# Optimization experiments

Measured on AMD Instinct MI355X. Metric: run time of the kernel, lower is better.

Reference implementation:

```python
import jax, jax.numpy as jnp
import numpy as np

N = 100000
E = 1600000
IN_C = 128
OUT_C = 32
HEADS = 4
NEG_SLOPE = 0.2


def setup_inputs() -> dict:
    key = jax.random.key(0)
    k1, k2, k3, k4, k5 = jax.random.split(key, 5)
    x = jax.random.normal(k1, (N, IN_C), dtype=jnp.float32)
    edge_index = jax.random.randint(k2, (2, E), 0, N, dtype=jnp.int64)
    # Xavier-ish scaled params
    W = jax.random.normal(k3, (OUT_C * HEADS, IN_C), dtype=jnp.float32) * (1.414 * np.sqrt(2.0 / (IN_C + OUT_C * HEADS)))
    att_l = jax.random.normal(k4, (1, HEADS, OUT_C), dtype=jnp.float32) * 0.1
    att_r = jax.random.normal(k5, (1, HEADS, OUT_C), dtype=jnp.float32) * 0.1
    bias = jnp.zeros((OUT_C * HEADS,), dtype=jnp.float32)
    return {"x": x, "edge_index": edge_index, "W": W, "att_l": att_l, "att_r": att_r, "bias": bias}


def reference(x, edge_index, W, att_l, att_r, bias):
    row, col = edge_index[0], edge_index[1]
    # per-node projection: [N, H, C]
    x_proj = (x @ W.T).reshape(N, HEADS, OUT_C)
    x_i = x_proj[row]          # [E, H, C] gather by source
    x_j = x_proj[col]          # [E, H, C] gather by target
    alpha = (x_i * att_l).sum(-1) + (x_j * att_r).sum(-1)   # [E, H]
    alpha = jnp.where(alpha >= 0, alpha, NEG_SLOPE * alpha)  # leaky_relu
    # edge softmax grouped by row (faithful: plain exp, eps=1e-16)
    alpha_exp = jnp.exp(alpha)
    denom = jax.ops.segment_sum(alpha_exp, row, num_segments=N)  # [N, H]
    alpha = alpha_exp / (denom[row] + 1e-16)
    # weighted scatter-add over all heads at once: [N, H, C]
    out = jax.ops.segment_sum(x_j * alpha[:, :, None], row, num_segments=N)
    out = out.reshape(N, HEADS * OUT_C) + bias
    return out
```

## Files before the change

### kernel.cpp

```cpp
#include <hip/hip_runtime.h>
#include <hip/hip_fp16.h>


constexpr float NEG_SLOPE = 0.2f;
constexpr int TILE_ROWS = 64;
constexpr int SLAB = 2048;
constexpr int EPB = 8192;
constexpr int NB_PAD = 2048;
constexpr int FBMAX = 256;

typedef __attribute__((ext_vector_type(8))) short short8;
typedef __attribute__((ext_vector_type(4))) float f32x4;

__device__ inline short f2bf(float f) {
    unsigned u = __float_as_uint(f);
    return (short)((u + 0x7fffu + ((u >> 16) & 1u)) >> 16);
}

__global__ __launch_bounds__(256) void k_prep(const float* __restrict__ W,
                                              const float* __restrict__ attl,
                                              const float* __restrict__ attr,
                                              short* __restrict__ Wa) {
    int blk = blockIdx.x;
    int t = threadIdx.x;
    if (blk < 64) {
        int i = blk * 256 + t;
        Wa[i] = f2bf(W[i]);
    } else if (blk == 64) {
        for (int s = t; s < 1024; s += 256) {
            int which = s >> 9;
            int h = (s >> 7) & 3;
            int k = s & 127;
            const float* att = which ? attr : attl;
            float acc = 0.f;
#pragma unroll 8
            for (int c = 0; c < 32; ++c)
                acc += att[h * 32 + c] * W[(h * 32 + c) * 128 + k];
            Wa[(128 + which * 4 + h) * 128 + k] = f2bf(acc);
        }
    } else {
        int i = (blk - 65) * 256 + t;
        if (i < 1024) Wa[136 * 128 + i] = 0;
    }
}

__global__ __launch_bounds__(512) void k_fill(const int* __restrict__ ei,
                                              unsigned int* __restrict__ slab,
                                              int* __restrict__ starts,
                                              int E, int NB) {
    __shared__ int s_hist[NB_PAD];
    __shared__ int s_cur[NB_PAD];
    __shared__ unsigned int s_stage[EPB];
    __shared__ int s_wsum[8];

    int fb = blockIdx.x;
    int t = threadIdx.x;
    int lane = t & 63, wv = t >> 6;
    int e0 = fb * EPB;
    int ecnt = min(EPB, E - e0);
    bool full = (ecnt == EPB) && ((E & 3) == 0);

    for (int i = t; i < NB_PAD; i += 512) s_hist[i] = 0;
    __syncthreads();

    const int* rows = ei;
    const int* cols = ei + E;

    if (full) {
        const int4* r4 = (const int4*)rows + (e0 >> 2);
#pragma unroll
        for (int k = 0; k < 4; ++k) {
            int4 ra = r4[k * 512 + t];
            atomicAdd(&s_hist[ra.x >> 6], 1);
            atomicAdd(&s_hist[ra.y >> 6], 1);
            atomicAdd(&s_hist[ra.z >> 6], 1);
            atomicAdd(&s_hist[ra.w >> 6], 1);
        }
    } else {
        for (int j = t; j < ecnt; j += 512)
            atomicAdd(&s_hist[rows[e0 + j] >> 6], 1);
    }
    __syncthreads();

    int b0 = t * 4;
    int c0 = s_hist[b0], c1 = s_hist[b0 + 1], c2 = s_hist[b0 + 2], c3 = s_hist[b0 + 3];
    int p = c0 + c1 + c2 + c3;
    int v = p;
#pragma unroll
    for (int off = 1; off < 64; off <<= 1) {
        int u = __shfl_up(v, off);
        if (lane >= off) v += u;
    }
    if (lane == 63) s_wsum[wv] = v;
    __syncthreads();
    if (t == 0) {
        int run = 0;
#pragma unroll
        for (int w = 0; w < 8; ++w) { int tmp = s_wsum[w]; s_wsum[w] = run; run += tmp; }
    }
    __syncthreads();
    int base = s_wsum[wv] + (v - p);
    int e1 = base + c0, e2 = e1 + c1, e3 = e2 + c2;
    s_hist[b0] = base; s_hist[b0 + 1] = e1; s_hist[b0 + 2] = e2; s_hist[b0 + 3] = e3;
    s_cur[b0] = base;  s_cur[b0 + 1] = e1;  s_cur[b0 + 2] = e2;  s_cur[b0 + 3] = e3;
    size_t sb = (size_t)fb * (NB + 1);
    if (b0 + 0 <= NB) starts[sb + b0 + 0] = base;
    if (b0 + 1 <= NB) starts[sb + b0 + 1] = e1;
    if (b0 + 2 <= NB) starts[sb + b0 + 2] = e2;
    if (b0 + 3 <= NB) starts[sb + b0 + 3] = e3;
    __syncthreads();

    if (full) {
        const int4* r4 = (const int4*)rows + (e0 >> 2);
        const int4* c4 = (const int4*)cols + (e0 >> 2);
#pragma unroll
        for (int k = 0; k < 4; ++k) {
            int4 ra = r4[k * 512 + t];
            int4 ca = c4[k * 512 + t];
            int pos;
            pos = atomicAdd(&s_cur[ra.x >> 6], 1);
            s_stage[pos] = ((unsigned int)ca.x << 6) | (unsigned int)(ra.x & 63);
            pos = atomicAdd(&s_cur[ra.y >> 6], 1);
            s_stage[pos] = ((unsigned int)ca.y << 6) | (unsigned int)(ra.y & 63);
            pos = atomicAdd(&s_cur[ra.z >> 6], 1);
            s_stage[pos] = ((unsigned int)ca.z << 6) | (unsigned int)(ra.z & 63);
            pos = atomicAdd(&s_cur[ra.w >> 6], 1);
            s_stage[pos] = ((unsigned int)ca.w << 6) | (unsigned int)(ra.w & 63);
        }
    } else {
        for (int j = t; j < ecnt; j += 512) {
            int rr = rows[e0 + j], cc = cols[e0 + j];
            int pos = atomicAdd(&s_cur[rr >> 6], 1);
            s_stage[pos] = ((unsigned int)cc << 6) | (unsigned int)(rr & 63);
        }
    }
    __syncthreads();

    uint4* dst = (uint4*)(slab + (size_t)fb * EPB);
    const uint4* src = (const uint4*)s_stage;
    int n4 = (ecnt + 3) >> 2;
    for (int i = t; i < n4; i += 512) dst[i] = src[i];
}

__global__ __launch_bounds__(256) void k_gemm(const float* __restrict__ x,
                                              const short* __restrict__ Wa,
                                              __half* __restrict__ xph,
                                              float* __restrict__ l,
                                              float* __restrict__ r,
                                              int N) {
    int t = threadIdx.x;
    int wave = t >> 6, lane = t & 63;
    int li = lane & 15, quad = lane >> 4;
    int base = blockIdx.x * 64 + wave * 16;

    f32x4 acc[9];
#pragma unroll
    for (int nt = 0; nt < 9; ++nt) acc[nt] = (f32x4){0.f, 0.f, 0.f, 0.f};

    int anode = base + li;
    bool avalid = anode < N;
    const float4* x4 = (const float4*)x;
    const short8* wb8 = (const short8*)Wa;

#pragma unroll
    for (int kc = 0; kc < 4; ++kc) {
        float4 p0 = make_float4(0.f, 0.f, 0.f, 0.f), p1 = p0;
        if (avalid) {
            p0 = x4[(size_t)anode * 32 + kc * 8 + quad * 2];
            p1 = x4[(size_t)anode * 32 + kc * 8 + quad * 2 + 1];
        }
        short8 a;
        a[0] = f2bf(p0.x); a[1] = f2bf(p0.y); a[2] = f2bf(p0.z); a[3] = f2bf(p0.w);
        a[4] = f2bf(p1.x); a[5] = f2bf(p1.y); a[6] = f2bf(p1.z); a[7] = f2bf(p1.w);
#pragma unroll
        for (int nt = 0; nt < 9; ++nt) {
            short8 b = wb8[(nt * 16 + li) * 16 + kc * 4 + quad];
            acc[nt] = __builtin_amdgcn_mfma_f32_16x16x32_bf16(a, b, acc[nt], 0, 0, 0);
        }
    }

#pragma unroll
    for (int j = 0; j < 4; ++j) {
        int node = base + quad * 4 + j;
        if (node >= N) continue;
#pragma unroll
        for (int nt = 0; nt < 8; ++nt)
            xph[(size_t)node * 128 + nt * 16 + li] = __float2half(acc[nt][j]);
        if (li < 4)      l[node * 4 + li] = acc[8][j];
        else if (li < 8) r[node * 4 + li - 4] = acc[8][j];
    }
}

__global__ __launch_bounds__(512) void k_tile(const int* __restrict__ starts,
                                              const unsigned int* __restrict__ slab,
                                              const float* __restrict__ l,
                                              const float* __restrict__ r,
                                              const __half* __restrict__ xph,
                                              const float* __restrict__ bias,
                                              float* __restrict__ out,
                                              int N, int NB, int FB) {
    __shared__ unsigned int s_packed[SLAB];
    __shared__ int s_col[SLAB];
    __shared__ int s_start[TILE_ROWS + 1];
    __shared__ int s_cursor[TILE_ROWS];
    __shared__ int s_cnt[TILE_ROWS];
    __shared__ int s_fbase[FBMAX];
    __shared__ int s_foff[FBMAX + 1];
    __shared__ int s_w4[4];

    int b = blockIdx.x;
    int base = b * TILE_ROWS;
    int t = threadIdx.x;
    int lane = t & 63, wv = t >> 6;

    if (t < TILE_ROWS) s_cnt[t] = 0;

    int myc = 0;
    if (t < FB) {
        const int* sp = starts + (size_t)t * (NB + 1) + b;
        int a0 = sp[0], a1 = sp[1];
        s_fbase[t] = a0;
        myc = a1 - a0;
    }
    int v = 0;
    if (t < 256) {
        v = myc;
#pragma unroll
        for (int off = 1; off < 64; off <<= 1) {
            int u = __shfl_up(v, off);
            if (lane >= off) v += u;
        }
        if (lane == 63) s_w4[wv] = v;
    }
    __syncthreads();
    if (t == 0) {
        int run = 0;
#pragma unroll
        for (int w = 0; w < 4; ++w) { int tmp = s_w4[w]; s_w4[w] = run; run += tmp; }
        s_foff[0] = 0;
    }
    __syncthreads();
    if (t < 256) s_foff[t + 1] = v + s_w4[wv];
    __syncthreads();
    int tot = s_foff[FB];
    if (tot > SLAB) tot = SLAB;

    for (int i = t; i < tot; i += 512) {
        int lo = 0, hi = FB;
        while (hi - lo > 1) {
            int mid = (lo + hi) >> 1;
            if (s_foff[mid] <= i) lo = mid; else hi = mid;
        }
        unsigned int p = slab[(size_t)lo * EPB + s_fbase[lo] + (i - s_foff[lo])];
        s_packed[i] = p;
        atomicAdd(&s_cnt[p & 63], 1);
    }
    __syncthreads();

    if (t < 64) {
        int c = s_cnt[t];
        int vv = c;
#pragma unroll
        for (int off = 1; off < 64; off <<= 1) {
            int u = __shfl_up(vv, off);
            if (t >= off) vv += u;
        }
        s_start[t + 1] = vv;
        if (t == 0) s_start[0] = 0;
        s_cursor[t] = vv - c;
    }
    __syncthreads();
    for (int i = t; i < tot; i += 512) {
        unsigned int p = s_packed[i];
        int pos = atomicAdd(&s_cursor[p & 63], 1);
        s_col[pos] = (int)(p >> 6);
    }
    __syncthreads();

    int quarter = lane >> 4;
    int li = lane & 15;
    int h = li >> 2;
    int rows = min(TILE_ROWS, N - base);
    const float4* xp4g = (const float4*)xph;

    float4 b0 = ((const float4*)bias)[2 * li];
    float4 b1 = ((const float4*)bias)[2 * li + 1];

    for (int rl = wv; rl < rows; rl += 8) {
        int s0 = s_start[rl], s1 = s_start[rl + 1];
        float lh = l[(base + rl) * 4 + h];
        float a0 = 0.f, a1 = 0.f, a2 = 0.f, a3 = 0.f;
        float a4 = 0.f, a5 = 0.f, a6 = 0.f, a7 = 0.f;
        float dsum = 0.f;
#pragma unroll 2
        for (int i = s0 + quarter; i < s1; i += 4) {
            int col = s_col[i];
            float rh = r[col * 4 + h];
            float a = lh + rh;
            a = a >= 0.f ? a : NEG_SLOPE * a;
            float w = __expf(a);
            float4 raw = xp4g[(size_t)col * 16 + li];
            __half2* hp = (__half2*)&raw;
            float2 f0 = __half22float2(hp[0]);
            float2 f1 = __half22float2(hp[1]);
            float2 f2 = __half22float2(hp[2]);
            float2 f3 = __half22float2(hp[3]);
            a0 += w * f0.x; a1 += w * f0.y;
            a2 += w * f1.x; a3 += w * f1.y;
            a4 += w * f2.x; a5 += w * f2.y;
            a6 += w * f3.x; a7 += w * f3.y;
            dsum += w;
        }
        a0 += __shfl_xor(a0, 16); a0 += __shfl_xor(a0, 32);
        a1 += __shfl_xor(a1, 16); a1 += __shfl_xor(a1, 32);
        a2 += __shfl_xor(a2, 16); a2 += __shfl_xor(a2, 32);
        a3 += __shfl_xor(a3, 16); a3 += __shfl_xor(a3, 32);
        a4 += __shfl_xor(a4, 16); a4 += __shfl_xor(a4, 32);
        a5 += __shfl_xor(a5, 16); a5 += __shfl_xor(a5, 32);
        a6 += __shfl_xor(a6, 16); a6 += __shfl_xor(a6, 32);
        a7 += __shfl_xor(a7, 16); a7 += __shfl_xor(a7, 32);
        dsum += __shfl_xor(dsum, 16); dsum += __shfl_xor(dsum, 32);
        if (quarter == 0) {
            float inv = 1.f / (dsum + 1e-16f);
            float4 o0, o1;
            o0.x = a0 * inv + b0.x; o0.y = a1 * inv + b0.y;
            o0.z = a2 * inv + b0.z; o0.w = a3 * inv + b0.w;
            o1.x = a4 * inv + b1.x; o1.y = a5 * inv + b1.y;
            o1.z = a6 * inv + b1.z; o1.w = a7 * inv + b1.w;
            ((float4*)out)[(size_t)(base + rl) * 32 + 2 * li] = o0;
            ((float4*)out)[(size_t)(base + rl) * 32 + 2 * li + 1] = o1;
        }
    }
}

extern "C" void kernel_launch(void* const* d_in, const int* in_sizes, int n_in,
                              void* d_out, int out_size, void* d_ws, size_t ws_size,
                              hipStream_t stream) {
    const float* x    = (const float*)d_in[0];
    const int*   ei   = (const int*)d_in[1];
    const float* W    = (const float*)d_in[2];
    const float* attl = (const float*)d_in[3];
    const float* attr = (const float*)d_in[4];
    const float* bias = (const float*)d_in[5];
    int N = in_sizes[0] / 128;
    int E = in_sizes[1] / 2;
    int NB = (N + TILE_ROWS - 1) / TILE_ROWS;
    int FB = (E + EPB - 1) / EPB;

    char* ws = (char*)d_ws;
    __half* xph = (__half*)ws;   ws += (size_t)N * 128 * 2;
    float* l    = (float*)ws;    ws += (size_t)N * 4 * 4;
    float* r    = (float*)ws;    ws += (size_t)N * 4 * 4;
    short* Wa   = (short*)ws;    ws += 144 * 128 * 2;
    int* starts = (int*)ws;      ws += (size_t)FB * (NB + 1) * 4;
    unsigned int* slab = (unsigned int*)ws; ws += (size_t)FB * EPB * 4;

    float* out = (float*)d_out;
    int GB = (N + 63) / 64;

    k_prep<<<69, 256, 0, stream>>>(W, attl, attr, Wa);
    k_fill<<<FB, 512, 0, stream>>>(ei, slab, starts, E, NB);
    k_gemm<<<GB, 256, 0, stream>>>(x, Wa, xph, l, r, N);
    k_tile<<<NB, 512, 0, stream>>>(starts, slab, l, r, xph, bias, out, N, NB, FB);
}
```

Baseline: 230.1 us.

## Stage GEMM weights in LDS and precompute per-edge softmax weights once per edge

The GEMM kernel now runs 512 threads per block, covering 128 nodes, and stages the 144x128 bf16 weight matrix into padded shared memory so the MFMA B-operand loads come from LDS instead of global memory. The tile kernel computes the four per-head exp weights once per edge during the bucketing pass. It stores them as fp16 in shared memory and accumulates the denominators with shared-memory atomics, so the inner gather loop no longer recomputes exp or reloads r once per head-lane group. The gather loop is also manually unrolled into two independent loads per iteration. In exchange, shared memory use rises (about 39KB in GEMM and an extra 16KB+ in the tile kernel), which may lower occupancy, and storing weights in fp16 slightly reduces precision.

```diff
diff --git a/kernel.cpp b/kernel.cpp
--- a/kernel.cpp
+++ b/kernel.cpp
@@ -142,16 +142,27 @@
     for (int i = t; i < n4; i += 512) dst[i] = src[i];
 }
 
-__global__ __launch_bounds__(256) void k_gemm(const float* __restrict__ x,
+__global__ __launch_bounds__(512) void k_gemm(const float* __restrict__ x,
                                               const short* __restrict__ Wa,
                                               __half* __restrict__ xph,
                                               float* __restrict__ l,
                                               float* __restrict__ r,
                                               int N) {
+    __shared__ short s_wa[144 * 136];
     int t = threadIdx.x;
+    {
+        const short8* g = (const short8*)Wa;
+        short8* s = (short8*)s_wa;
+        for (int i = t; i < 144 * 16; i += 512) {
+            int row = i >> 4, k8 = i & 15;
+            s[row * 17 + k8] = g[i];
+        }
+    }
+    __syncthreads();
+
     int wave = t >> 6, lane = t & 63;
     int li = lane & 15, quad = lane >> 4;
-    int base = blockIdx.x * 64 + wave * 16;
+    int base = blockIdx.x * 128 + wave * 16;
 
     f32x4 acc[9];
 #pragma unroll
@@ -160,7 +171,7 @@
     int anode = base + li;
     bool avalid = anode < N;
     const float4* x4 = (const float4*)x;
-    const short8* wb8 = (const short8*)Wa;
+    const short8* wb8 = (const short8*)s_wa;
 
 #pragma unroll
     for (int kc = 0; kc < 4; ++kc) {
@@ -174,7 +185,7 @@
         a[4] = f2bf(p1.x); a[5] = f2bf(p1.y); a[6] = f2bf(p1.z); a[7] = f2bf(p1.w);
 #pragma unroll
         for (int nt = 0; nt < 9; ++nt) {
-            short8 b = wb8[(nt * 16 + li) * 16 + kc * 4 + quad];
+            short8 b = wb8[(nt * 16 + li) * 17 + kc * 4 + quad];
             acc[nt] = __builtin_amdgcn_mfma_f32_16x16x32_bf16(a, b, acc[nt], 0, 0, 0);
         }
     }
@@ -201,6 +212,9 @@
                                               int N, int NB, int FB) {
     __shared__ unsigned int s_packed[SLAB];
     __shared__ int s_col[SLAB];
+    __shared__ __half s_w[SLAB * 4];
+    __shared__ float s_dsum[TILE_ROWS * 4];
+    __shared__ float s_l[TILE_ROWS * 4];
     __shared__ int s_start[TILE_ROWS + 1];
     __shared__ int s_cursor[TILE_ROWS];
     __shared__ int s_cnt[TILE_ROWS];
@@ -212,8 +226,11 @@
     int base = b * TILE_ROWS;
     int t = threadIdx.x;
     int lane = t & 63, wv = t >> 6;
+    int rows = min(TILE_ROWS, N - base);
 
     if (t < TILE_ROWS) s_cnt[t] = 0;
+    if (t < TILE_ROWS * 4) s_dsum[t] = 0.f;
+    if (t < rows * 4) s_l[t] = l[base * 4 + t];
 
     int myc = 0;
     if (t < FB) {
@@ -270,17 +287,34 @@
         s_cursor[t] = vv - c;
     }
     __syncthreads();
+
     for (int i = t; i < tot; i += 512) {
         unsigned int p = s_packed[i];
-        int pos = atomicAdd(&s_cursor[p & 63], 1);
-        s_col[pos] = (int)(p >> 6);
+        int row = (int)(p & 63);
+        int col = (int)(p >> 6);
+        int pos = atomicAdd(&s_cursor[row], 1);
+        s_col[pos] = col;
+        float4 rv = ((const float4*)r)[col];
+        float4 lv = ((const float4*)s_l)[row];
+        float w0 = lv.x + rv.x, w1 = lv.y + rv.y;
+        float w2 = lv.z + rv.z, w3 = lv.w + rv.w;
+        w0 = w0 >= 0.f ? w0 : NEG_SLOPE * w0;
+        w1 = w1 >= 0.f ? w1 : NEG_SLOPE * w1;
+        w2 = w2 >= 0.f ? w2 : NEG_SLOPE * w2;
+        w3 = w3 >= 0.f ? w3 : NEG_SLOPE * w3;
+        w0 = __expf(w0); w1 = __expf(w1); w2 = __expf(w2); w3 = __expf(w3);
+        ((__half2*)s_w)[pos * 2]     = __floats2half2_rn(w0, w1);
+        ((__half2*)s_w)[pos * 2 + 1] = __floats2half2_rn(w2, w3);
+        atomicAdd(&s_dsum[row * 4 + 0], w0);
+        atomicAdd(&s_dsum[row * 4 + 1], w1);
+        atomicAdd(&s_dsum[row * 4 + 2], w2);
+        atomicAdd(&s_dsum[row * 4 + 3], w3);
     }
     __syncthreads();
 
     int quarter = lane >> 4;
     int li = lane & 15;
     int h = li >> 2;
-    int rows = min(TILE_ROWS, N - base);
     const float4* xp4g = (const float4*)xph;
 
     float4 b0 = ((const float4*)bias)[2 * li];
@@ -288,28 +322,39 @@
 
     for (int rl = wv; rl < rows; rl += 8) {
         int s0 = s_start[rl], s1 = s_start[rl + 1];
-        float lh = l[(base + rl) * 4 + h];
         float a0 = 0.f, a1 = 0.f, a2 = 0.f, a3 = 0.f;
         float a4 = 0.f, a5 = 0.f, a6 = 0.f, a7 = 0.f;
-        float dsum = 0.f;
-#pragma unroll 2
-        for (int i = s0 + quarter; i < s1; i += 4) {
-            int col = s_col[i];
-            float rh = r[col * 4 + h];
-            float a = lh + rh;
-            a = a >= 0.f ? a : NEG_SLOPE * a;
-            float w = __expf(a);
-            float4 raw = xp4g[(size_t)col * 16 + li];
-            __half2* hp = (__half2*)&raw;
-            float2 f0 = __half22float2(hp[0]);
-            float2 f1 = __half22float2(hp[1]);
-            float2 f2 = __half22float2(hp[2]);
-            float2 f3 = __half22float2(hp[3]);
-            a0 += w * f0.x; a1 += w * f0.y;
-            a2 += w * f1.x; a3 += w * f1.y;
-            a4 += w * f2.x; a5 += w * f2.y;
-            a6 += w * f3.x; a7 += w * f3.y;
-            dsum += w;
+        for (int i = s0 + quarter; i < s1; i += 8) {
+            int iB = i + 4;
+            bool hB = iB < s1;
+            int colA = s_col[i];
+            float wA = __half2float(s_w[i * 4 + h]);
+            int colB = hB ? s_col[iB] : colA;
+            float wB = hB ? __half2float(s_w[iB * 4 + h]) : 0.f;
+            float4 rawA = xp4g[(size_t)colA * 16 + li];
+            float4 rawB = xp4g[(size_t)colB * 16 + li];
+            {
+                __half2* hp = (__half2*)&rawA;
+                float2 f0 = __half22float2(hp[0]);
+                float2 f1 = __half22float2(hp[1]);
+                float2 f2 = __half22float2(hp[2]);
+                float2 f3 = __half22float2(hp[3]);
+                a0 += wA * f0.x; a1 += wA * f0.y;
+                a2 += wA * f1.x; a3 += wA * f1.y;
+                a4 += wA * f2.x; a5 += wA * f2.y;
+                a6 += wA * f3.x; a7 += wA * f3.y;
+            }
+            {
+                __half2* hp = (__half2*)&rawB;
+                float2 f0 = __half22float2(hp[0]);
+                float2 f1 = __half22float2(hp[1]);
+                float2 f2 = __half22float2(hp[2]);
+                float2 f3 = __half22float2(hp[3]);
+                a0 += wB * f0.x; a1 += wB * f0.y;
+                a2 += wB * f1.x; a3 += wB * f1.y;
+                a4 += wB * f2.x; a5 += wB * f2.y;
+                a6 += wB * f3.x; a7 += wB * f3.y;
+            }
         }
         a0 += __shfl_xor(a0, 16); a0 += __shfl_xor(a0, 32);
         a1 += __shfl_xor(a1, 16); a1 += __shfl_xor(a1, 32);
@@ -319,9 +364,8 @@
         a5 += __shfl_xor(a5, 16); a5 += __shfl_xor(a5, 32);
         a6 += __shfl_xor(a6, 16); a6 += __shfl_xor(a6, 32);
         a7 += __shfl_xor(a7, 16); a7 += __shfl_xor(a7, 32);
-        dsum += __shfl_xor(dsum, 16); dsum += __shfl_xor(dsum, 32);
         if (quarter == 0) {
-            float inv = 1.f / (dsum + 1e-16f);
+            float inv = 1.f / (s_dsum[rl * 4 + h] + 1e-16f);
             float4 o0, o1;
             o0.x = a0 * inv + b0.x; o0.y = a1 * inv + b0.y;
             o0.z = a2 * inv + b0.z; o0.w = a3 * inv + b0.w;
@@ -356,10 +400,10 @@
     unsigned int* slab = (unsigned int*)ws; ws += (size_t)FB * EPB * 4;
 
     float* out = (float*)d_out;
-    int GB = (N + 63) / 64;
+    int GB = (N + 127) / 128;
 
     k_prep<<<69, 256, 0, stream>>>(W, attl, attr, Wa);
     k_fill<<<FB, 512, 0, stream>>>(ei, slab, starts, E, NB);
-    k_gemm<<<GB, 256, 0, stream>>>(x, Wa, xph, l, r, N);
+    k_gemm<<<GB, 512, 0, stream>>>(x, Wa, xph, l, r, N);
     k_tile<<<NB, 512, 0, stream>>>(starts, slab, l, r, xph, bias, out, N, NB, FB);
 }
```

New measurement: 224.6 us. 1.02x faster.
